# Performance work log

Hardware: AMD Instinct MI355X
Metric: run time of the kernel (lower is better)

## Reference

```python
import jax, jax.numpy as jnp
import numpy as np

N, E = 50000, 800000
IN_DIM, HID, OUT_DIM = 128, 64, 64
H1, H2 = 4, 2
LRELU_SLOPE = 0.2
LN_EPS = 1e-5


def _glorot(key, shape):
    fan = shape[0] + shape[-1]
    lim = float(np.sqrt(6.0 / fan))
    return jax.random.uniform(key, shape, jnp.float32, -lim, lim)


def setup_inputs() -> dict:
    key = jax.random.key(0)
    ks = jax.random.split(key, 12)
    x = jax.random.normal(ks[0], (N, IN_DIM), jnp.float32)
    edge_index = jax.random.randint(ks[1], (2, E), 0, N, jnp.int64)
    return {
        "x": x,
        "edge_index": edge_index,
        # layer 1: GATConv(128 -> 64, heads=4, concat=True)
        "W1": _glorot(ks[2], (IN_DIM, H1 * HID)),
        "att_src1": _glorot(ks[3], (H1, HID)),
        "att_dst1": _glorot(ks[4], (H1, HID)),
        "b1": jnp.zeros((H1 * HID,), jnp.float32),
        # LayerNorm(256)
        "ln_w": jnp.ones((H1 * HID,), jnp.float32),
        "ln_b": jnp.zeros((H1 * HID,), jnp.float32),
        # layer 2: GATConv(256 -> 64, heads=2, concat=False)
        "W2": _glorot(ks[5], (H1 * HID, H2 * OUT_DIM)),
        "att_src2": _glorot(ks[6], (H2, OUT_DIM)),
        "att_dst2": _glorot(ks[7], (H2, OUT_DIM)),
        "b2": jnp.zeros((OUT_DIM,), jnp.float32),
    }


def gat_layer(x, src, dst, W, a_src, a_dst, bias, heads, out_ch, concat):
    n = x.shape[0]
    h = (x @ W).reshape(n, heads, out_ch)                 # [N,H,C]
    al_s = jnp.einsum("nhc,hc->nh", h, a_src)             # [N,H]
    al_d = jnp.einsum("nhc,hc->nh", h, a_dst)
    e = jax.nn.leaky_relu(al_s[src] + al_d[dst], LRELU_SLOPE)  # [E,H]
    # segment softmax over incoming edges of each dst node
    m = jax.ops.segment_max(e, dst, num_segments=n)
    e = jnp.exp(e - m[dst])
    denom = jax.ops.segment_sum(e, dst, num_segments=n)
    alpha = e / denom[dst]                                # [E,H]
    msg = h[src] * alpha[:, :, None]                      # [E,H,C]
    out = jax.ops.segment_sum(msg, dst, num_segments=n)   # [N,H,C]
    out = out.reshape(n, heads * out_ch) if concat else out.mean(axis=1)
    return out + bias


def layer_norm(x, w, b):
    mu = x.mean(axis=-1, keepdims=True)
    var = ((x - mu) ** 2).mean(axis=-1, keepdims=True)
    return (x - mu) * jax.lax.rsqrt(var + LN_EPS) * w + b


def reference(x, edge_index, W1, att_src1, att_dst1, b1, ln_w, ln_b,
              W2, att_src2, att_dst2, b2):
    # PyG GATConv adds self-loops by default
    loops = jnp.arange(N, dtype=edge_index.dtype)
    src = jnp.concatenate([edge_index[0], loops])
    dst = jnp.concatenate([edge_index[1], loops])
    h = gat_layer(x, src, dst, W1, att_src1, att_dst1, b1, H1, HID, True)
    h = layer_norm(h, ln_w, ln_b)
    h = jax.nn.elu(h)
    # dropout is identity in eval mode
    h = gat_layer(h, src, dst, W2, att_src2, att_dst2, b2, H2, OUT_DIM, False)
    return h
```

## Files before the change

kernel.cpp:

```cpp
#include <hip/hip_runtime.h>
#include <hip/hip_bf16.h>
#include <math.h>

#define IN_DIM  128
#define HID     64
#define H1      4
#define H2      2
#define OUT_DIM 64
#define D1      256
#define D2      128
#define LRELU   0.2f
#define LN_EPS  1e-5f

using short8 = __attribute__((ext_vector_type(8))) short;
using f32x4  = __attribute__((ext_vector_type(4))) float;

static __device__ __forceinline__ unsigned short f2bf_bits(float f)
{
    __hip_bfloat16 b = __float2bfloat16(f);
    return *reinterpret_cast<unsigned short*>(&b);
}
static __device__ __forceinline__ float2 unpack_bf2(unsigned int p)
{
    float2 r;
    r.x = __uint_as_float(p << 16);
    r.y = __uint_as_float(p & 0xffff0000u);
    return r;
}
static __device__ __forceinline__ unsigned int pack_bf2(float x, float y)
{
    return (unsigned int)f2bf_bits(x) | ((unsigned int)f2bf_bits(y) << 16);
}

template<int H>
static __device__ __forceinline__ float edge_w(
    const float* __restrict__ al_s, int src, float ad, int h)
{
    float v = al_s[(size_t)src * H + h] + ad;
    v = v > 0.f ? v : LRELU * v;
    return __expf(v);
}

static __device__ __forceinline__ int detect_i64(const int* __restrict__ ei)
{
    int any_odd_nonzero = 0;
    #pragma unroll
    for (int k = 1; k < 16; k += 2) any_odd_nonzero |= (ei[k] != 0);
    return any_odd_nonzero ? 0 : 1;
}

__global__ __launch_bounds__(256) void hist_kernel(
    const int* __restrict__ ei, int E, int* __restrict__ deg)
{
    const int i64f = detect_i64(ei);
    int e = blockIdx.x * 256 + threadIdx.x;
    if (e >= E) return;
    int dst = i64f ? ei[2 * ((size_t)E + e)] : ei[E + e];
    atomicAdd(&deg[dst], 1);
}

__global__ __launch_bounds__(256) void scan_partial(
    const int* __restrict__ deg, int N, int* __restrict__ bsum)
{
    __shared__ int s[256];
    int i = blockIdx.x * 256 + threadIdx.x;
    s[threadIdx.x] = (i < N) ? deg[i] : 0;
    __syncthreads();
    for (int st = 128; st > 0; st >>= 1) {
        if (threadIdx.x < st) s[threadIdx.x] += s[threadIdx.x + st];
        __syncthreads();
    }
    if (threadIdx.x == 0) bsum[blockIdx.x] = s[0];
}

__global__ __launch_bounds__(256) void scan_top(
    int* __restrict__ bsum, int B, int* __restrict__ totalp)
{
    __shared__ int s[256];
    int v = (threadIdx.x < B) ? bsum[threadIdx.x] : 0;
    s[threadIdx.x] = v;
    __syncthreads();
    for (int st = 1; st < 256; st <<= 1) {
        int t = (threadIdx.x >= st) ? s[threadIdx.x - st] : 0;
        __syncthreads();
        s[threadIdx.x] += t;
        __syncthreads();
    }
    if (threadIdx.x < B) bsum[threadIdx.x] = s[threadIdx.x] - v;
    if (threadIdx.x == 255) *totalp = s[255];
}

__global__ __launch_bounds__(256) void scan_final(
    const int* __restrict__ deg, const int* __restrict__ bsum, int N,
    int* __restrict__ rowptr, int* __restrict__ cursor)
{
    __shared__ int s[256];
    int i = blockIdx.x * 256 + threadIdx.x;
    int v = (i < N) ? deg[i] : 0;
    s[threadIdx.x] = v;
    __syncthreads();
    for (int st = 1; st < 256; st <<= 1) {
        int t = (threadIdx.x >= st) ? s[threadIdx.x - st] : 0;
        __syncthreads();
        s[threadIdx.x] += t;
        __syncthreads();
    }
    int excl = s[threadIdx.x] - v + bsum[blockIdx.x];
    if (i < N) { rowptr[i] = excl; cursor[i] = excl; }
}

__global__ __launch_bounds__(256) void fill_kernel(
    const int* __restrict__ ei, int E,
    int* __restrict__ cursor, int* __restrict__ csr_src)
{
    const int i64f = detect_i64(ei);
    int e = blockIdx.x * 256 + threadIdx.x;
    if (e >= E) return;
    int src, dst;
    if (i64f) { src = ei[2 * (size_t)e]; dst = ei[2 * ((size_t)E + e)]; }
    else      { src = ei[e];             dst = ei[E + e]; }
    int pos = atomicAdd(&cursor[dst], 1);
    csr_src[pos] = src;
}

__global__ __launch_bounds__(256) void conv_weights(
    const float* __restrict__ W1, const float* __restrict__ W2,
    unsigned short* __restrict__ Wp1, unsigned short* __restrict__ Wp2)
{
    int tid = blockIdx.x * 256 + threadIdx.x;
    if (tid < 32768) {
        int j = tid & 7, l = (tid >> 3) & 63, rest = tid >> 9;
        int s = rest & 15, t = rest >> 4;
        int k = t * 32 + (l >> 4) * 8 + j, col = s * 16 + (l & 15);
        Wp1[tid] = f2bf_bits(W1[k * D1 + col]);
    } else {
        int id = tid - 32768;
        int j = id & 7, l = (id >> 3) & 63, rest = id >> 9;
        int s = rest & 7, t = rest >> 3;
        int k = t * 32 + (l >> 4) * 8 + j, col = s * 16 + (l & 15);
        Wp2[id] = f2bf_bits(W2[k * D2 + col]);
    }
}

__global__ __launch_bounds__(256) void gemm1_mfma(
    const float* __restrict__ x, const unsigned short* __restrict__ Wp,
    const float* __restrict__ att_s, const float* __restrict__ att_d,
    unsigned short* __restrict__ h1b,
    float* __restrict__ al_s, float* __restrict__ al_d, int N)
{
    __shared__ __align__(16) unsigned short As[16 * 136];
    const int tid = threadIdx.x;
    const int n0 = blockIdx.x * 16;
    const int l = tid & 63, w = tid >> 6;

    #pragma unroll
    for (int it = 0; it < 2; ++it) {
        int ch = tid + it * 256;
        int r = ch >> 5, c4 = (ch & 31) * 4;
        int row = n0 + r;
        float4 v = (row < N) ? ((const float4*)x)[(size_t)row * 32 + (c4 >> 2)]
                             : make_float4(0.f, 0.f, 0.f, 0.f);
        ushort4 pk = make_ushort4(f2bf_bits(v.x), f2bf_bits(v.y),
                                  f2bf_bits(v.z), f2bf_bits(v.w));
        *(ushort4*)&As[r * 136 + c4] = pk;
    }

    short8 bfr[4][4];
    #pragma unroll
    for (int t = 0; t < 4; ++t)
        #pragma unroll
        for (int p = 0; p < 4; ++p)
            bfr[t][p] = ((const short8*)Wp)[(t * 16 + (w * 4 + p)) * 64 + l];

    __syncthreads();

    f32x4 acc[4] = {{0.f,0.f,0.f,0.f},{0.f,0.f,0.f,0.f},
                    {0.f,0.f,0.f,0.f},{0.f,0.f,0.f,0.f}};
    #pragma unroll
    for (int t = 0; t < 4; ++t) {
        short8 a = *(const short8*)&As[(l & 15) * 136 + t * 32 + (l >> 4) * 8];
        #pragma unroll
        for (int p = 0; p < 4; ++p)
            acc[p] = __builtin_amdgcn_mfma_f32_16x16x32_bf16(a, bfr[t][p], acc[p], 0, 0, 0);
    }

    const int colbase = w * 64 + (l & 15);
    const int rowbase = n0 + (l >> 4) * 4;
    #pragma unroll
    for (int p = 0; p < 4; ++p) {
        int col = colbase + p * 16;
        #pragma unroll
        for (int r = 0; r < 4; ++r) {
            int row = rowbase + r;
            if (row < N) h1b[(size_t)row * D1 + col] = f2bf_bits(acc[p][r]);
        }
    }

    float as_p[4], ad_p[4];
    #pragma unroll
    for (int p = 0; p < 4; ++p) {
        as_p[p] = att_s[colbase + p * 16];
        ad_p[p] = att_d[colbase + p * 16];
    }
    #pragma unroll
    for (int r = 0; r < 4; ++r) {
        float ps = acc[0][r] * as_p[0] + acc[1][r] * as_p[1]
                 + acc[2][r] * as_p[2] + acc[3][r] * as_p[3];
        float pd = acc[0][r] * ad_p[0] + acc[1][r] * ad_p[1]
                 + acc[2][r] * ad_p[2] + acc[3][r] * ad_p[3];
        #pragma unroll
        for (int off = 8; off > 0; off >>= 1) {
            ps += __shfl_down(ps, off);
            pd += __shfl_down(pd, off);
        }
        int row = rowbase + r;
        if ((l & 15) == 0 && row < N) {
            al_s[(size_t)row * H1 + w] = ps;
            al_d[(size_t)row * H1 + w] = pd;
        }
    }
}

__global__ __launch_bounds__(256) void gemm2_mfma(
    const unsigned short* __restrict__ hmidb, const unsigned short* __restrict__ Wp,
    const float* __restrict__ att_s, const float* __restrict__ att_d,
    unsigned short* __restrict__ h2b,
    float* __restrict__ al_s, float* __restrict__ al_d, int N)
{
    __shared__ __align__(16) unsigned short As[16 * 264];
    __shared__ float psL[4][16], pdL[4][16];
    const int tid = threadIdx.x;
    const int n0 = blockIdx.x * 16;
    const int l = tid & 63, w = tid >> 6;

    const short8 zero8 = {0,0,0,0,0,0,0,0};
    #pragma unroll
    for (int it = 0; it < 2; ++it) {
        int ch = tid + it * 256;
        int r = ch >> 5, c8 = (ch & 31) * 8;
        int row = n0 + r;
        short8 v = (row < N) ? ((const short8*)hmidb)[(size_t)row * 32 + (ch & 31)] : zero8;
        *(short8*)&As[r * 264 + c8] = v;
    }

    short8 bfr[8][2];
    #pragma unroll
    for (int t = 0; t < 8; ++t)
        #pragma unroll
        for (int q = 0; q < 2; ++q)
            bfr[t][q] = ((const short8*)Wp)[(t * 8 + (w * 2 + q)) * 64 + l];

    __syncthreads();

    f32x4 acc[2] = {{0.f,0.f,0.f,0.f},{0.f,0.f,0.f,0.f}};
    #pragma unroll
    for (int t = 0; t < 8; ++t) {
        short8 a = *(const short8*)&As[(l & 15) * 264 + t * 32 + (l >> 4) * 8];
        #pragma unroll
        for (int q = 0; q < 2; ++q)
            acc[q] = __builtin_amdgcn_mfma_f32_16x16x32_bf16(a, bfr[t][q], acc[q], 0, 0, 0);
    }

    const int colbase = w * 32 + (l & 15);
    const int rowbase = n0 + (l >> 4) * 4;
    #pragma unroll
    for (int q = 0; q < 2; ++q) {
        int col = colbase + q * 16;
        #pragma unroll
        for (int r = 0; r < 4; ++r) {
            int row = rowbase + r;
            if (row < N) h2b[(size_t)row * D2 + col] = f2bf_bits(acc[q][r]);
        }
    }

    float as_q[2], ad_q[2];
    #pragma unroll
    for (int q = 0; q < 2; ++q) {
        as_q[q] = att_s[colbase + q * 16];
        ad_q[q] = att_d[colbase + q * 16];
    }
    #pragma unroll
    for (int r = 0; r < 4; ++r) {
        float ps = acc[0][r] * as_q[0] + acc[1][r] * as_q[1];
        float pd = acc[0][r] * ad_q[0] + acc[1][r] * ad_q[1];
        #pragma unroll
        for (int off = 8; off > 0; off >>= 1) {
            ps += __shfl_down(ps, off);
            pd += __shfl_down(pd, off);
        }
        if ((l & 15) == 0) {
            psL[w][(l >> 4) * 4 + r] = ps;
            pdL[w][(l >> 4) * 4 + r] = pd;
        }
    }
    __syncthreads();
    if (tid < 32) {
        int rl = tid & 15, hh = tid >> 4;
        int row = n0 + rl;
        if (row < N) {
            al_s[(size_t)row * H2 + hh] = psL[2*hh][rl] + psL[2*hh+1][rl];
            al_d[(size_t)row * H2 + hh] = pdL[2*hh][rl] + pdL[2*hh+1][rl];
        }
    }
}

__global__ __launch_bounds__(64) void agg1_kernel(
    const int* __restrict__ rowptr, const int* __restrict__ csr_src,
    const uint2* __restrict__ h1p,
    const float* __restrict__ al_s, const float* __restrict__ al_d,
    const float* __restrict__ b1,
    const float* __restrict__ ln_w, const float* __restrict__ ln_b,
    uint2* __restrict__ hmidp, int N)
{
    const int n = blockIdx.x;
    const int t = threadIdx.x;
    const int h = t >> 4;
    const float ad = al_d[(size_t)n * H1 + h];

    float a0[4] = {0.f,0.f,0.f,0.f}, a1[4] = {0.f,0.f,0.f,0.f};
    float a2[4] = {0.f,0.f,0.f,0.f}, a3[4] = {0.f,0.f,0.f,0.f};
    float dn0, dn1 = 0.f, dn2 = 0.f, dn3 = 0.f;

    {
        float w = edge_w<H1>(al_s, n, ad, h);
        uint2 p = h1p[(size_t)n * 64 + t];
        float2 va = unpack_bf2(p.x), vb = unpack_bf2(p.y);
        a0[0] = w * va.x; a0[1] = w * va.y; a0[2] = w * vb.x; a0[3] = w * vb.y;
        dn0 = w;
    }

    const int beg = rowptr[n], end = rowptr[n + 1];
    int i = beg;
    for (; i + 4 <= end; i += 4) {
        int s0 = csr_src[i], s1 = csr_src[i+1], s2 = csr_src[i+2], s3 = csr_src[i+3];
        uint2 p0 = h1p[(size_t)s0 * 64 + t];
        uint2 p1 = h1p[(size_t)s1 * 64 + t];
        uint2 p2 = h1p[(size_t)s2 * 64 + t];
        uint2 p3 = h1p[(size_t)s3 * 64 + t];
        float w0 = edge_w<H1>(al_s, s0, ad, h);
        float w1 = edge_w<H1>(al_s, s1, ad, h);
        float w2 = edge_w<H1>(al_s, s2, ad, h);
        float w3 = edge_w<H1>(al_s, s3, ad, h);
        float2 v0a = unpack_bf2(p0.x), v0b = unpack_bf2(p0.y);
        float2 v1a = unpack_bf2(p1.x), v1b = unpack_bf2(p1.y);
        float2 v2a = unpack_bf2(p2.x), v2b = unpack_bf2(p2.y);
        float2 v3a = unpack_bf2(p3.x), v3b = unpack_bf2(p3.y);
        a0[0] += w0 * v0a.x; a0[1] += w0 * v0a.y; a0[2] += w0 * v0b.x; a0[3] += w0 * v0b.y; dn0 += w0;
        a1[0] += w1 * v1a.x; a1[1] += w1 * v1a.y; a1[2] += w1 * v1b.x; a1[3] += w1 * v1b.y; dn1 += w1;
        a2[0] += w2 * v2a.x; a2[1] += w2 * v2a.y; a2[2] += w2 * v2b.x; a2[3] += w2 * v2b.y; dn2 += w2;
        a3[0] += w3 * v3a.x; a3[1] += w3 * v3a.y; a3[2] += w3 * v3b.x; a3[3] += w3 * v3b.y; dn3 += w3;
    }
    for (; i < end; ++i) {
        int s0 = csr_src[i];
        uint2 p0 = h1p[(size_t)s0 * 64 + t];
        float w0 = edge_w<H1>(al_s, s0, ad, h);
        float2 v0a = unpack_bf2(p0.x), v0b = unpack_bf2(p0.y);
        a0[0] += w0 * v0a.x; a0[1] += w0 * v0a.y; a0[2] += w0 * v0b.x; a0[3] += w0 * v0b.y; dn0 += w0;
    }

    const float inv = 1.f / ((dn0 + dn1) + (dn2 + dn3));
    float4 bb = ((const float4*)b1)[t];
    float v[4];
    v[0] = ((a0[0]+a1[0]) + (a2[0]+a3[0])) * inv + bb.x;
    v[1] = ((a0[1]+a1[1]) + (a2[1]+a3[1])) * inv + bb.y;
    v[2] = ((a0[2]+a1[2]) + (a2[2]+a3[2])) * inv + bb.z;
    v[3] = ((a0[3]+a1[3]) + (a2[3]+a3[3])) * inv + bb.w;

    float s  = (v[0]+v[1]) + (v[2]+v[3]);
    float s2 = (v[0]*v[0]+v[1]*v[1]) + (v[2]*v[2]+v[3]*v[3]);
    #pragma unroll
    for (int off = 32; off > 0; off >>= 1) {
        s  += __shfl_down(s,  off);
        s2 += __shfl_down(s2, off);
    }
    const float mu   = __shfl(s,  0) * (1.f / 256.f);
    const float ex2  = __shfl(s2, 0) * (1.f / 256.f);
    const float rstd = rsqrtf(ex2 - mu * mu + LN_EPS);
    float4 lw = ((const float4*)ln_w)[t];
    float4 lb = ((const float4*)ln_b)[t];
    float y0 = (v[0] - mu) * rstd * lw.x + lb.x;
    float y1 = (v[1] - mu) * rstd * lw.y + lb.y;
    float y2 = (v[2] - mu) * rstd * lw.z + lb.z;
    float y3 = (v[3] - mu) * rstd * lw.w + lb.w;
    y0 = y0 > 0.f ? y0 : (__expf(y0) - 1.f);
    y1 = y1 > 0.f ? y1 : (__expf(y1) - 1.f);
    y2 = y2 > 0.f ? y2 : (__expf(y2) - 1.f);
    y3 = y3 > 0.f ? y3 : (__expf(y3) - 1.f);
    uint2 outp;
    outp.x = pack_bf2(y0, y1);
    outp.y = pack_bf2(y2, y3);
    hmidp[(size_t)n * 64 + t] = outp;
}

__global__ __launch_bounds__(64) void agg2_kernel(
    const int* __restrict__ rowptr, const int* __restrict__ csr_src,
    const unsigned int* __restrict__ h2p,
    const float* __restrict__ al_s, const float* __restrict__ al_d,
    const float* __restrict__ b2,
    float* __restrict__ out, int N)
{
    const int n = blockIdx.x;
    const int t = threadIdx.x;
    const int h = t >> 5;
    const float ad = al_d[(size_t)n * H2 + h];

    const float ws = edge_w<H2>(al_s, n, ad, h);
    float2 hv = unpack_bf2(h2p[(size_t)n * 64 + t]);
    float ax0 = ws * hv.x, ay0 = ws * hv.y, dn0 = ws;
    float ax1 = 0.f, ay1 = 0.f, dn1 = 0.f;
    float ax2 = 0.f, ay2 = 0.f, dn2 = 0.f;
    float ax3 = 0.f, ay3 = 0.f, dn3 = 0.f;

    const int beg = rowptr[n], end = rowptr[n + 1];
    int i = beg;
    for (; i + 4 <= end; i += 4) {
        int s0 = csr_src[i], s1 = csr_src[i+1], s2 = csr_src[i+2], s3 = csr_src[i+3];
        unsigned int p0 = h2p[(size_t)s0 * 64 + t];
        unsigned int p1 = h2p[(size_t)s1 * 64 + t];
        unsigned int p2 = h2p[(size_t)s2 * 64 + t];
        unsigned int p3 = h2p[(size_t)s3 * 64 + t];
        float w0 = edge_w<H2>(al_s, s0, ad, h);
        float w1 = edge_w<H2>(al_s, s1, ad, h);
        float w2 = edge_w<H2>(al_s, s2, ad, h);
        float w3 = edge_w<H2>(al_s, s3, ad, h);
        float2 v0 = unpack_bf2(p0), v1 = unpack_bf2(p1);
        float2 v2 = unpack_bf2(p2), v3 = unpack_bf2(p3);
        ax0 += w0 * v0.x; ay0 += w0 * v0.y; dn0 += w0;
        ax1 += w1 * v1.x; ay1 += w1 * v1.y; dn1 += w1;
        ax2 += w2 * v2.x; ay2 += w2 * v2.y; dn2 += w2;
        ax3 += w3 * v3.x; ay3 += w3 * v3.y; dn3 += w3;
    }
    for (; i < end; ++i) {
        int s0 = csr_src[i];
        unsigned int p0 = h2p[(size_t)s0 * 64 + t];
        float w0 = edge_w<H2>(al_s, s0, ad, h);
        float2 v0 = unpack_bf2(p0);
        ax0 += w0 * v0.x; ay0 += w0 * v0.y; dn0 += w0;
    }

    const float inv = 1.f / ((dn0 + dn1) + (dn2 + dn3));
    const float vx = ((ax0 + ax1) + (ax2 + ax3)) * inv;
    const float vy = ((ay0 + ay1) + (ay2 + ay3)) * inv;

    __shared__ float sv[128];
    sv[2 * t]     = vx;
    sv[2 * t + 1] = vy;
    __syncthreads();
    out[(size_t)n * OUT_DIM + t] = 0.5f * (sv[t] + sv[64 + t]) + b2[t];
}

extern "C" void kernel_launch(void* const* d_in, const int* in_sizes, int n_in,
                              void* d_out, int out_size, void* d_ws, size_t ws_size,
                              hipStream_t stream)
{
    const float* x   = (const float*)d_in[0];
    const int*   ei  = (const int*)d_in[1];
    const float* W1  = (const float*)d_in[2];
    const float* as1 = (const float*)d_in[3];
    const float* ad1 = (const float*)d_in[4];
    const float* b1  = (const float*)d_in[5];
    const float* lnw = (const float*)d_in[6];
    const float* lnb = (const float*)d_in[7];
    const float* W2  = (const float*)d_in[8];
    const float* as2 = (const float*)d_in[9];
    const float* ad2 = (const float*)d_in[10];
    const float* b2  = (const float*)d_in[11];

    const int N = in_sizes[0] / IN_DIM;
    const int E = in_sizes[1] / 2;

    char* ws = (char*)d_ws;
    const size_t szH1b = (size_t)N * D1 * sizeof(unsigned short);
    unsigned short* h1b   = (unsigned short*)(ws);
    unsigned short* hmidb = (unsigned short*)(ws + szH1b);
    unsigned short* Wp1   = (unsigned short*)(ws + 2 * szH1b);
    unsigned short* Wp2   = Wp1 + 32768;
    float* al_s1 = (float*)(Wp2 + 32768);
    float* al_d1 = al_s1 + (size_t)N * H1;
    float* al_s2 = al_d1 + (size_t)N * H1;
    float* al_d2 = al_s2 + (size_t)N * H2;
    int* deg     = (int*)(al_d2 + (size_t)N * H2);
    int* rowptr  = deg + (N + 1);
    int* cursor  = rowptr + (N + 1);
    int* csr_src = cursor + (N + 1);
    int* bsum    = csr_src + E;
    unsigned short* h2b = h1b;

    hipMemsetAsync(deg, 0, (size_t)(N + 1) * sizeof(int), stream);

    const int edgeBlocks = (E + 255) / 256;
    const int scanBlocks = (N + 255) / 256;
    const int tileBlocks = (N + 15) / 16;

    conv_weights<<<256, 256, 0, stream>>>(W1, W2, Wp1, Wp2);
    hist_kernel<<<edgeBlocks, 256, 0, stream>>>(ei, E, deg);
    scan_partial<<<scanBlocks, 256, 0, stream>>>(deg, N, bsum);
    scan_top<<<1, 256, 0, stream>>>(bsum, scanBlocks, rowptr + N);
    scan_final<<<scanBlocks, 256, 0, stream>>>(deg, bsum, N, rowptr, cursor);
    fill_kernel<<<edgeBlocks, 256, 0, stream>>>(ei, E, cursor, csr_src);

    gemm1_mfma<<<tileBlocks, 256, 0, stream>>>(x, Wp1, as1, ad1, h1b, al_s1, al_d1, N);
    agg1_kernel<<<N, 64, 0, stream>>>(rowptr, csr_src, (const uint2*)h1b,
                                      al_s1, al_d1, b1, lnw, lnb,
                                      (uint2*)hmidb, N);
    gemm2_mfma<<<tileBlocks, 256, 0, stream>>>(hmidb, Wp2, as2, ad2, h2b, al_s2, al_d2, N);
    agg2_kernel<<<N, 64, 0, stream>>>(rowptr, csr_src, (const unsigned int*)h2b,
                                      al_s2, al_d2, b2, (float*)d_out, N);
}
```

Measured before the change: 318.2 us.

## Merge setup kernels and deepen edge-loop unrolling in aggregation kernels

```diff
diff --git a/kernel.cpp b/kernel.cpp
--- a/kernel.cpp
+++ b/kernel.cpp
@@ -49,14 +49,33 @@
     return any_odd_nonzero ? 0 : 1;
 }
 
-__global__ __launch_bounds__(256) void hist_kernel(
+__global__ __launch_bounds__(256) void conv_hist_kernel(
+    const float* __restrict__ W1, const float* __restrict__ W2,
+    unsigned short* __restrict__ Wp1, unsigned short* __restrict__ Wp2,
     const int* __restrict__ ei, int E, int* __restrict__ deg)
 {
-    const int i64f = detect_i64(ei);
-    int e = blockIdx.x * 256 + threadIdx.x;
-    if (e >= E) return;
-    int dst = i64f ? ei[2 * ((size_t)E + e)] : ei[E + e];
-    atomicAdd(&deg[dst], 1);
+    const int bid = blockIdx.x;
+    if (bid < 256) {
+        int tid = bid * 256 + threadIdx.x;
+        if (tid < 32768) {
+            int j = tid & 7, l = (tid >> 3) & 63, rest = tid >> 9;
+            int s = rest & 15, t = rest >> 4;
+            int k = t * 32 + (l >> 4) * 8 + j, col = s * 16 + (l & 15);
+            Wp1[tid] = f2bf_bits(W1[k * D1 + col]);
+        } else {
+            int id = tid - 32768;
+            int j = id & 7, l = (id >> 3) & 63, rest = id >> 9;
+            int s = rest & 7, t = rest >> 3;
+            int k = t * 32 + (l >> 4) * 8 + j, col = s * 16 + (l & 15);
+            Wp2[id] = f2bf_bits(W2[k * D2 + col]);
+        }
+    } else {
+        const int i64f = detect_i64(ei);
+        int e = (bid - 256) * 256 + threadIdx.x;
+        if (e >= E) return;
+        int dst = i64f ? ei[2 * ((size_t)E + e)] : ei[E + e];
+        atomicAdd(&deg[dst], 1);
+    }
 }
 
 __global__ __launch_bounds__(256) void scan_partial(
@@ -73,11 +92,24 @@
     if (threadIdx.x == 0) bsum[blockIdx.x] = s[0];
 }
 
-__global__ __launch_bounds__(256) void scan_top(
-    int* __restrict__ bsum, int B, int* __restrict__ totalp)
-{
+__global__ __launch_bounds__(256) void scan_final(
+    const int* __restrict__ deg, const int* __restrict__ bsum, int B, int N, int E,
+    int* __restrict__ rowptr, int* __restrict__ cursor)
+{
+    __shared__ int sb[256];
     __shared__ int s[256];
-    int v = (threadIdx.x < B) ? bsum[threadIdx.x] : 0;
+    sb[threadIdx.x] = (threadIdx.x < B) ? bsum[threadIdx.x] : 0;
+    __syncthreads();
+    for (int st = 1; st < 256; st <<= 1) {
+        int t = (threadIdx.x >= st) ? sb[threadIdx.x - st] : 0;
+        __syncthreads();
+        sb[threadIdx.x] += t;
+        __syncthreads();
+    }
+    const int blockOff = (blockIdx.x == 0) ? 0 : sb[blockIdx.x - 1];
+
+    int i = blockIdx.x * 256 + threadIdx.x;
+    int v = (i < N) ? deg[i] : 0;
     s[threadIdx.x] = v;
     __syncthreads();
     for (int st = 1; st < 256; st <<= 1) {
@@ -86,27 +118,9 @@
         s[threadIdx.x] += t;
         __syncthreads();
     }
-    if (threadIdx.x < B) bsum[threadIdx.x] = s[threadIdx.x] - v;
-    if (threadIdx.x == 255) *totalp = s[255];
-}
-
-__global__ __launch_bounds__(256) void scan_final(
-    const int* __restrict__ deg, const int* __restrict__ bsum, int N,
-    int* __restrict__ rowptr, int* __restrict__ cursor)
-{
-    __shared__ int s[256];
-    int i = blockIdx.x * 256 + threadIdx.x;
-    int v = (i < N) ? deg[i] : 0;
-    s[threadIdx.x] = v;
-    __syncthreads();
-    for (int st = 1; st < 256; st <<= 1) {
-        int t = (threadIdx.x >= st) ? s[threadIdx.x - st] : 0;
-        __syncthreads();
-        s[threadIdx.x] += t;
-        __syncthreads();
-    }
-    int excl = s[threadIdx.x] - v + bsum[blockIdx.x];
+    int excl = s[threadIdx.x] - v + blockOff;
     if (i < N) { rowptr[i] = excl; cursor[i] = excl; }
+    if (blockIdx.x == 0 && threadIdx.x == 0) rowptr[N] = E;
 }
 
 __global__ __launch_bounds__(256) void fill_kernel(
@@ -121,25 +135,6 @@
     else      { src = ei[e];             dst = ei[E + e]; }
     int pos = atomicAdd(&cursor[dst], 1);
     csr_src[pos] = src;
-}
-
-__global__ __launch_bounds__(256) void conv_weights(
-    const float* __restrict__ W1, const float* __restrict__ W2,
-    unsigned short* __restrict__ Wp1, unsigned short* __restrict__ Wp2)
-{
-    int tid = blockIdx.x * 256 + threadIdx.x;
-    if (tid < 32768) {
-        int j = tid & 7, l = (tid >> 3) & 63, rest = tid >> 9;
-        int s = rest & 15, t = rest >> 4;
-        int k = t * 32 + (l >> 4) * 8 + j, col = s * 16 + (l & 15);
-        Wp1[tid] = f2bf_bits(W1[k * D1 + col]);
-    } else {
-        int id = tid - 32768;
-        int j = id & 7, l = (id >> 3) & 63, rest = id >> 9;
-        int s = rest & 7, t = rest >> 3;
-        int k = t * 32 + (l >> 4) * 8 + j, col = s * 16 + (l & 15);
-        Wp2[id] = f2bf_bits(W2[k * D2 + col]);
-    }
 }
 
 __global__ __launch_bounds__(256) void gemm1_mfma(
@@ -331,32 +326,29 @@
 
     const int beg = rowptr[n], end = rowptr[n + 1];
     int i = beg;
+
+#define LOADE1(k) int s##k = csr_src[i + k]; \
+                  uint2 p##k = h1p[(size_t)s##k * 64 + t]; \
+                  float w##k = edge_w<H1>(al_s, s##k, ad, h);
+#define ACC1(A, D, k) { float2 va = unpack_bf2(p##k.x), vb = unpack_bf2(p##k.y); \
+                        A[0] += w##k * va.x; A[1] += w##k * va.y; \
+                        A[2] += w##k * vb.x; A[3] += w##k * vb.y; D += w##k; }
+
+    for (; i + 8 <= end; i += 8) {
+        LOADE1(0) LOADE1(1) LOADE1(2) LOADE1(3)
+        LOADE1(4) LOADE1(5) LOADE1(6) LOADE1(7)
+        ACC1(a0, dn0, 0) ACC1(a1, dn1, 1) ACC1(a2, dn2, 2) ACC1(a3, dn3, 3)
+        ACC1(a0, dn0, 4) ACC1(a1, dn1, 5) ACC1(a2, dn2, 6) ACC1(a3, dn3, 7)
+    }
     for (; i + 4 <= end; i += 4) {
-        int s0 = csr_src[i], s1 = csr_src[i+1], s2 = csr_src[i+2], s3 = csr_src[i+3];
-        uint2 p0 = h1p[(size_t)s0 * 64 + t];
-        uint2 p1 = h1p[(size_t)s1 * 64 + t];
-        uint2 p2 = h1p[(size_t)s2 * 64 + t];
-        uint2 p3 = h1p[(size_t)s3 * 64 + t];
-        float w0 = edge_w<H1>(al_s, s0, ad, h);
-        float w1 = edge_w<H1>(al_s, s1, ad, h);
-        float w2 = edge_w<H1>(al_s, s2, ad, h);
-        float w3 = edge_w<H1>(al_s, s3, ad, h);
-        float2 v0a = unpack_bf2(p0.x), v0b = unpack_bf2(p0.y);
-        float2 v1a = unpack_bf2(p1.x), v1b = unpack_bf2(p1.y);
-        float2 v2a = unpack_bf2(p2.x), v2b = unpack_bf2(p2.y);
-        float2 v3a = unpack_bf2(p3.x), v3b = unpack_bf2(p3.y);
-        a0[0] += w0 * v0a.x; a0[1] += w0 * v0a.y; a0[2] += w0 * v0b.x; a0[3] += w0 * v0b.y; dn0 += w0;
-        a1[0] += w1 * v1a.x; a1[1] += w1 * v1a.y; a1[2] += w1 * v1b.x; a1[3] += w1 * v1b.y; dn1 += w1;
-        a2[0] += w2 * v2a.x; a2[1] += w2 * v2a.y; a2[2] += w2 * v2b.x; a2[3] += w2 * v2b.y; dn2 += w2;
-        a3[0] += w3 * v3a.x; a3[1] += w3 * v3a.y; a3[2] += w3 * v3b.x; a3[3] += w3 * v3b.y; dn3 += w3;
+        LOADE1(0) LOADE1(1) LOADE1(2) LOADE1(3)
+        ACC1(a0, dn0, 0) ACC1(a1, dn1, 1) ACC1(a2, dn2, 2) ACC1(a3, dn3, 3)
     }
     for (; i < end; ++i) {
-        int s0 = csr_src[i];
-        uint2 p0 = h1p[(size_t)s0 * 64 + t];
-        float w0 = edge_w<H1>(al_s, s0, ad, h);
-        float2 v0a = unpack_bf2(p0.x), v0b = unpack_bf2(p0.y);
-        a0[0] += w0 * v0a.x; a0[1] += w0 * v0a.y; a0[2] += w0 * v0b.x; a0[3] += w0 * v0b.y; dn0 += w0;
-    }
+        LOADE1(0) ACC1(a0, dn0, 0)
+    }
+#undef LOADE1
+#undef ACC1
 
     const float inv = 1.f / ((dn0 + dn1) + (dn2 + dn3));
     float4 bb = ((const float4*)b1)[t];
@@ -404,39 +396,43 @@
     const int h = t >> 5;
     const float ad = al_d[(size_t)n * H2 + h];
 
-    const float ws = edge_w<H2>(al_s, n, ad, h);
-    float2 hv = unpack_bf2(h2p[(size_t)n * 64 + t]);
-    float ax0 = ws * hv.x, ay0 = ws * hv.y, dn0 = ws;
+    float ax0, ay0, dn0;
     float ax1 = 0.f, ay1 = 0.f, dn1 = 0.f;
     float ax2 = 0.f, ay2 = 0.f, dn2 = 0.f;
     float ax3 = 0.f, ay3 = 0.f, dn3 = 0.f;
+    {
+        float w = edge_w<H2>(al_s, n, ad, h);
+        float2 hv = unpack_bf2(h2p[(size_t)n * 64 + t]);
+        ax0 = w * hv.x; ay0 = w * hv.y; dn0 = w;
+    }
 
     const int beg = rowptr[n], end = rowptr[n + 1];
     int i = beg;
+
+#define LOADE2(k) int s##k = csr_src[i + k]; \
+                  unsigned int p##k = h2p[(size_t)s##k * 64 + t]; \
+                  float w##k = edge_w<H2>(al_s, s##k, ad, h);
+#define ACC2(AX, AY, D, k) { float2 vv = unpack_bf2(p##k); \
+                             AX += w##k * vv.x; AY += w##k * vv.y; D += w##k; }
+
+    for (; i + 8 <= end; i += 8) {
+        LOADE2(0) LOADE2(1) LOADE2(2) LOADE2(3)
+        LOADE2(4) LOADE2(5) LOADE2(6) LOADE2(7)
+        ACC2(ax0, ay0, dn0, 0) ACC2(ax1, ay1, dn1, 1)
+        ACC2(ax2, ay2, dn2, 2) ACC2(ax3, ay3, dn3, 3)
+        ACC2(ax0, ay0, dn0, 4) ACC2(ax1, ay1, dn1, 5)
+        ACC2(ax2, ay2, dn2, 6) ACC2(ax3, ay3, dn3, 7)
+    }
     for (; i + 4 <= end; i += 4) {
-        int s0 = csr_src[i], s1 = csr_src[i+1], s2 = csr_src[i+2], s3 = csr_src[i+3];
-        unsigned int p0 = h2p[(size_t)s0 * 64 + t];
-        unsigned int p1 = h2p[(size_t)s1 * 64 + t];
-        unsigned int p2 = h2p[(size_t)s2 * 64 + t];
-        unsigned int p3 = h2p[(size_t)s3 * 64 + t];
-        float w0 = edge_w<H2>(al_s, s0, ad, h);
-        float w1 = edge_w<H2>(al_s, s1, ad, h);
-        float w2 = edge_w<H2>(al_s, s2, ad, h);
-        float w3 = edge_w<H2>(al_s, s3, ad, h);
-        float2 v0 = unpack_bf2(p0), v1 = unpack_bf2(p1);
-        float2 v2 = unpack_bf2(p2), v3 = unpack_bf2(p3);
-        ax0 += w0 * v0.x; ay0 += w0 * v0.y; dn0 += w0;
-        ax1 += w1 * v1.x; ay1 += w1 * v1.y; dn1 += w1;
-        ax2 += w2 * v2.x; ay2 += w2 * v2.y; dn2 += w2;
-        ax3 += w3 * v3.x; ay3 += w3 * v3.y; dn3 += w3;
+        LOADE2(0) LOADE2(1) LOADE2(2) LOADE2(3)
+        ACC2(ax0, ay0, dn0, 0) ACC2(ax1, ay1, dn1, 1)
+        ACC2(ax2, ay2, dn2, 2) ACC2(ax3, ay3, dn3, 3)
     }
     for (; i < end; ++i) {
-        int s0 = csr_src[i];
-        unsigned int p0 = h2p[(size_t)s0 * 64 + t];
-        float w0 = edge_w<H2>(al_s, s0, ad, h);
-        float2 v0 = unpack_bf2(p0);
-        ax0 += w0 * v0.x; ay0 += w0 * v0.y; dn0 += w0;
-    }
+        LOADE2(0) ACC2(ax0, ay0, dn0, 0)
+    }
+#undef LOADE2
+#undef ACC2
 
     const float inv = 1.f / ((dn0 + dn1) + (dn2 + dn3));
     const float vx = ((ax0 + ax1) + (ax2 + ax3)) * inv;
@@ -492,11 +488,9 @@
     const int scanBlocks = (N + 255) / 256;
     const int tileBlocks = (N + 15) / 16;
 
-    conv_weights<<<256, 256, 0, stream>>>(W1, W2, Wp1, Wp2);
-    hist_kernel<<<edgeBlocks, 256, 0, stream>>>(ei, E, deg);
+    conv_hist_kernel<<<256 + edgeBlocks, 256, 0, stream>>>(W1, W2, Wp1, Wp2, ei, E, deg);
     scan_partial<<<scanBlocks, 256, 0, stream>>>(deg, N, bsum);
-    scan_top<<<1, 256, 0, stream>>>(bsum, scanBlocks, rowptr + N);
-    scan_final<<<scanBlocks, 256, 0, stream>>>(deg, bsum, N, rowptr, cursor);
+    scan_final<<<scanBlocks, 256, 0, stream>>>(deg, bsum, scanBlocks, N, E, rowptr, cursor);
     fill_kernel<<<edgeBlocks, 256, 0, stream>>>(ei, E, cursor, csr_src);
 
     gemm1_mfma<<<tileBlocks, 256, 0, stream>>>(x, Wp1, as1, ad1, h1b, al_s1, al_d1, N);
```

Result: no change. 314.0 us (-1.3%).
